# Kernel tuning notes

Measured on AMD Instinct MI355X. Metric: run time of the kernel, lower is better.

## Reference

```python
import jax, jax.numpy as jnp
import numpy as np

HEAD_DIM = 32
KERNEL = 3
DILATION = 2
PAD = DILATION * (KERNEL - 1) // 2  # 'same' padding for dilated window
SCALE = HEAD_DIM ** -0.5


def _unfold_windows(x):
    """x: [B, d, H, W] -> [B, d, k*k, H, W] dilated local windows.
    Matches torch nn.Unfold ordering: kernel row-major (i outer, j inner)."""
    B, d, H, W = x.shape
    xp = jnp.pad(x, ((0, 0), (0, 0), (PAD, PAD), (PAD, PAD)))
    taps = [xp[:, :, i * DILATION:i * DILATION + H, j * DILATION:j * DILATION + W]
            for i in range(KERNEL) for j in range(KERNEL)]  # fixed 9-tap loop
    return jnp.stack(taps, axis=2)


def setup_inputs() -> dict:
    key = jax.random.key(0)
    kq, kk, kv = jax.random.split(key, 3)
    shape = (16, 32, 128, 128)
    return {
        "q": jax.random.normal(kq, shape, dtype=jnp.float32),
        "k": jax.random.normal(kk, shape, dtype=jnp.float32),
        "v": jax.random.normal(kv, shape, dtype=jnp.float32),
    }


def reference(q, k, v):
    # k,v windows: [B, d, n, H, W] with n = kernel_size**2
    kw = _unfold_windows(k)
    vw = _unfold_windows(v)
    # per-pixel 1xN attention: scores [B, n, H, W]
    attn = jnp.einsum('bdhw,bdnhw->bnhw', q, kw) * SCALE
    attn = jax.nn.softmax(attn, axis=1)
    # weighted sum over window taps -> [B, d, H, W]
    return jnp.einsum('bnhw,bdnhw->bdhw', attn, vw)
```

## Files before the change

kernel.cpp:

```cpp
#include <hip/hip_runtime.h>


#define BB 16
#define HD 32
#define HH 128
#define WW 128
#define PLANE (HH * WW)
#define CHUNK 4

__global__ __launch_bounds__(128) void dilate_attn_kernel(
    const float* __restrict__ q,
    const float* __restrict__ k,
    const float* __restrict__ v,
    float* __restrict__ out)
{
    const int w   = threadIdx.x;
    const int bid = blockIdx.x;
    const int rowid = (bid & 7) * 256 + (bid >> 3);
    const int h = rowid & (HH - 1);
    const int b = rowid >> 7;

    const size_t base = ((size_t)b * HD) * PLANE + (size_t)h * WW + w;

    const int  dlo = (w >= 2)      ? -2      : -w;
    const int  dhi = (w <= WW - 3) ?  2      : (WW - 1 - w);
    const int  rlo = (h >= 2)      ? -2 * WW : 0;
    const int  rhi = (h <= HH - 3) ?  2 * WW : 0;
    const bool wlo = (w >= 2), whi = (w <= WW - 3);
    const bool hlo = (h >= 2), hhi = (h <= HH - 3);

    int off[9];
    off[0] = rlo + dlo; off[1] = rlo; off[2] = rlo + dhi;
    off[3] = dlo;       off[4] = 0;   off[5] = dhi;
    off[6] = rhi + dlo; off[7] = rhi; off[8] = rhi + dhi;

    const bool tv[9] = { hlo && wlo, hlo, hlo && whi,
                         wlo,        true, whi,
                         hhi && wlo, hhi, hhi && whi };

    float s[9];
    #pragma unroll
    for (int n = 0; n < 9; ++n) s[n] = 0.f;

    const float* qp = q + base;
    const float* kp = k + base;

    for (int dc = 0; dc < HD; dc += CHUNK) {
        float qreg[CHUNK];
        float kreg[CHUNK][9];
        #pragma unroll
        for (int u = 0; u < CHUNK; ++u) {
            const float* kc = kp + (size_t)(dc + u) * PLANE;
            qreg[u] = qp[(size_t)(dc + u) * PLANE];
            #pragma unroll
            for (int n = 0; n < 9; ++n) kreg[u][n] = kc[off[n]];
        }
        #pragma unroll
        for (int u = 0; u < CHUNK; ++u) {
            #pragma unroll
            for (int n = 0; n < 9; ++n)
                s[n] = fmaf(qreg[u], kreg[u][n], s[n]);
        }
    }

    #pragma unroll
    for (int n = 0; n < 9; ++n) if (!tv[n]) s[n] = 0.f;

    const float scale = 0.17677669529663687f;
    float m = -3.4e38f;
    #pragma unroll
    for (int n = 0; n < 9; ++n) { s[n] *= scale; m = fmaxf(m, s[n]); }
    float sum = 0.f;
    #pragma unroll
    for (int n = 0; n < 9; ++n) { s[n] = __expf(s[n] - m); sum += s[n]; }
    const float inv = 1.f / sum;
    #pragma unroll
    for (int n = 0; n < 9; ++n) s[n] *= inv;

    #pragma unroll
    for (int n = 0; n < 9; ++n) if (!tv[n]) s[n] = 0.f;

    const float* vp = v + base;
    float*       op = out + base;

    for (int dc = 0; dc < HD; dc += CHUNK) {
        float vreg[CHUNK][9];
        #pragma unroll
        for (int u = 0; u < CHUNK; ++u) {
            const float* vc = vp + (size_t)(dc + u) * PLANE;
            #pragma unroll
            for (int n = 0; n < 9; ++n) vreg[u][n] = vc[off[n]];
        }
        #pragma unroll
        for (int u = 0; u < CHUNK; ++u) {
            float acc = 0.f;
            #pragma unroll
            for (int n = 0; n < 9; ++n)
                acc = fmaf(s[n], vreg[u][n], acc);
            op[(size_t)(dc + u) * PLANE] = acc;
        }
    }
}

extern "C" void kernel_launch(void* const* d_in, const int* in_sizes, int n_in,
                              void* d_out, int out_size, void* d_ws, size_t ws_size,
                              hipStream_t stream) {
    const float* q = (const float*)d_in[0];
    const float* k = (const float*)d_in[1];
    const float* v = (const float*)d_in[2];
    float* out = (float*)d_out;

    dim3 grid(BB * HH);
    dim3 block(WW);
    dilate_attn_kernel<<<grid, block, 0, stream>>>(q, k, v, out);
}
```

Baseline: 34.31 us.

## Stage K/V row tiles in shared memory for multi-row blocks

Each block now handles four image rows with 512 threads and stages an 8-row halo strip of K and then V into LDS in channel chunks, using float4 global loads. Every thread reads its 9 window taps from shared memory, and Q is preloaded into registers for all channels. This replaces the many redundant global/L2 gathers per pixel, since the halo overlap is shared within a block. The cost is LDS traffic, two barriers per chunk and fewer, larger blocks (512 blocks in the grid). Halo rows outside the image are clamped and their taps masked as before.

Measured after the change: 33.25 us. -3.1%, faster.

```diff
diff --git a/kernel.cpp b/kernel.cpp
--- a/kernel.cpp
+++ b/kernel.cpp
@@ -6,61 +6,85 @@
 #define HH 128
 #define WW 128
 #define PLANE (HH * WW)
-#define CHUNK 4
+#define TH 4
+#define SR 8
+#define DC 8
+#define NCH (HD / DC)
+#define NT 512
 
-__global__ __launch_bounds__(128) void dilate_attn_kernel(
+__global__ __launch_bounds__(NT) void dilate_attn_kernel(
     const float* __restrict__ q,
     const float* __restrict__ k,
     const float* __restrict__ v,
     float* __restrict__ out)
 {
-    const int w   = threadIdx.x;
+    __shared__ float sm[DC * SR * WW];
+
+    const int tid = threadIdx.x;
     const int bid = blockIdx.x;
-    const int rowid = (bid & 7) * 256 + (bid >> 3);
-    const int h = rowid & (HH - 1);
-    const int b = rowid >> 7;
+    const int tile = (bid & 7) * 64 + (bid >> 3);
+    const int b  = tile >> 5;
+    const int r0 = (tile & 31) * TH;
 
-    const size_t base = ((size_t)b * HD) * PLANE + (size_t)h * WW + w;
+    const int lr = tid >> 7;
+    const int w  = tid & (WW - 1);
 
-    const int  dlo = (w >= 2)      ? -2      : -w;
-    const int  dhi = (w <= WW - 3) ?  2      : (WW - 1 - w);
-    const int  rlo = (h >= 2)      ? -2 * WW : 0;
-    const int  rhi = (h <= HH - 3) ?  2 * WW : 0;
+    const size_t bbase = (size_t)b * HD * PLANE;
+    const int pix = (r0 + lr) * WW + w;
+
+    const int  dlo = (w >= 2)      ? -2 : -w;
+    const int  dhi = (w <= WW - 3) ?  2 : (WW - 1 - w);
     const bool wlo = (w >= 2), whi = (w <= WW - 3);
+    const int  h   = r0 + lr;
     const bool hlo = (h >= 2), hhi = (h <= HH - 3);
-
-    int off[9];
-    off[0] = rlo + dlo; off[1] = rlo; off[2] = rlo + dhi;
-    off[3] = dlo;       off[4] = 0;   off[5] = dhi;
-    off[6] = rhi + dlo; off[7] = rhi; off[8] = rhi + dhi;
-
     const bool tv[9] = { hlo && wlo, hlo, hlo && whi,
                          wlo,        true, whi,
                          hhi && wlo, hhi, hhi && whi };
+
+    float qreg[HD];
+    #pragma unroll
+    for (int d = 0; d < HD; ++d)
+        qreg[d] = q[bbase + (size_t)d * PLANE + pix];
 
     float s[9];
     #pragma unroll
     for (int n = 0; n < 9; ++n) s[n] = 0.f;
 
-    const float* qp = q + base;
-    const float* kp = k + base;
-
-    for (int dc = 0; dc < HD; dc += CHUNK) {
-        float qreg[CHUNK];
-        float kreg[CHUNK][9];
+    for (int c = 0; c < NCH; ++c) {
+        {
+            float4 tmp[4];
+            int    la[4];
+            #pragma unroll
+            for (int j = 0; j < 4; ++j) {
+                const int i   = tid + j * NT;
+                const int u   = i >> 8;
+                const int rem = i & 255;
+                const int row = rem >> 5;
+                const int w4  = (rem & 31) << 2;
+                int gr = r0 - 2 + row;
+                gr = gr < 0 ? 0 : (gr > HH - 1 ? HH - 1 : gr);
+                tmp[j] = *(const float4*)(k + bbase + (size_t)(c * DC + u) * PLANE
+                                          + (size_t)gr * WW + w4);
+                la[j] = u * (SR * WW) + row * WW + w4;
+            }
+            #pragma unroll
+            for (int j = 0; j < 4; ++j)
+                *(float4*)(sm + la[j]) = tmp[j];
+        }
+        __syncthreads();
         #pragma unroll
-        for (int u = 0; u < CHUNK; ++u) {
-            const float* kc = kp + (size_t)(dc + u) * PLANE;
-            qreg[u] = qp[(size_t)(dc + u) * PLANE];
+        for (int u = 0; u < DC; ++u) {
+            const float  qd = qreg[c * DC + u];
+            const float* rp0 = sm + u * (SR * WW) + lr * WW + w;
             #pragma unroll
-            for (int n = 0; n < 9; ++n) kreg[u][n] = kc[off[n]];
+            for (int ti = 0; ti < 3; ++ti) {
+                const float* rp = rp0 + ti * 2 * WW;
+                s[ti * 3 + 0] = fmaf(qd, rp[dlo], s[ti * 3 + 0]);
+                s[ti * 3 + 1] = fmaf(qd, rp[0],   s[ti * 3 + 1]);
+                s[ti * 3 + 2] = fmaf(qd, rp[dhi], s[ti * 3 + 2]);
+            }
         }
-        #pragma unroll
-        for (int u = 0; u < CHUNK; ++u) {
-            #pragma unroll
-            for (int n = 0; n < 9; ++n)
-                s[n] = fmaf(qreg[u], kreg[u][n], s[n]);
-        }
+        __syncthreads();
     }
 
     #pragma unroll
@@ -80,25 +104,42 @@
     #pragma unroll
     for (int n = 0; n < 9; ++n) if (!tv[n]) s[n] = 0.f;
 
-    const float* vp = v + base;
-    float*       op = out + base;
-
-    for (int dc = 0; dc < HD; dc += CHUNK) {
-        float vreg[CHUNK][9];
+    for (int c = 0; c < NCH; ++c) {
+        {
+            float4 tmp[4];
+            int    la[4];
+            #pragma unroll
+            for (int j = 0; j < 4; ++j) {
+                const int i   = tid + j * NT;
+                const int u   = i >> 8;
+                const int rem = i & 255;
+                const int row = rem >> 5;
+                const int w4  = (rem & 31) << 2;
+                int gr = r0 - 2 + row;
+                gr = gr < 0 ? 0 : (gr > HH - 1 ? HH - 1 : gr);
+                tmp[j] = *(const float4*)(v + bbase + (size_t)(c * DC + u) * PLANE
+                                          + (size_t)gr * WW + w4);
+                la[j] = u * (SR * WW) + row * WW + w4;
+            }
+            #pragma unroll
+            for (int j = 0; j < 4; ++j)
+                *(float4*)(sm + la[j]) = tmp[j];
+        }
+        __syncthreads();
         #pragma unroll
-        for (int u = 0; u < CHUNK; ++u) {
-            const float* vc = vp + (size_t)(dc + u) * PLANE;
-            #pragma unroll
-            for (int n = 0; n < 9; ++n) vreg[u][n] = vc[off[n]];
-        }
-        #pragma unroll
-        for (int u = 0; u < CHUNK; ++u) {
+        for (int u = 0; u < DC; ++u) {
+            const float* rp0 = sm + u * (SR * WW) + lr * WW + w;
             float acc = 0.f;
             #pragma unroll
-            for (int n = 0; n < 9; ++n)
-                acc = fmaf(s[n], vreg[u][n], acc);
-            op[(size_t)(dc + u) * PLANE] = acc;
+            for (int ti = 0; ti < 3; ++ti) {
+                const float* rp = rp0 + ti * 2 * WW;
+                acc = fmaf(s[ti * 3 + 0], rp[dlo], acc);
+                acc = fmaf(s[ti * 3 + 1], rp[0],   acc);
+                acc = fmaf(s[ti * 3 + 2], rp[dhi], acc);
+            }
+            out[bbase + (size_t)(c * DC + u) * PLANE + pix] = acc;
         }
+        __syncthreads();
     }
 }
 
@@ -110,7 +151,7 @@
     const float* v = (const float*)d_in[2];
     float* out = (float*)d_out;
 
-    dim3 grid(BB * HH);
-    dim3 block(WW);
+    dim3 grid(BB * HH / TH);
+    dim3 block(NT);
     dilate_attn_kernel<<<grid, block, 0, stream>>>(q, k, v, out);
 }
```

## Process two pixels per thread with float2 loads and split head dim across half-waves

Applied to the files above, without the earlier changes.

Each thread now handles two adjacent pixels using float2 loads and stores for q, k, v and out. The 32-channel head dimension is split between the two half-waves of a 64-lane wavefront, and the partial scores are combined with a cross-lane xor shuffle. Each 256-thread block covers two rows, so the grid is halved. The aim is to cut the number of load instructions and the per-pixel address overhead in this memory-bound kernel, and to give each thread more independent work. In exchange it needs more registers per thread, and the shuffle adds a reduction step.

Result: slower. 48.55 us (+41.5%).

```diff
diff --git a/kernel.cpp b/kernel.cpp
--- a/kernel.cpp
+++ b/kernel.cpp
@@ -7,97 +7,134 @@
 #define WW 128
 #define PLANE (HH * WW)
 #define CHUNK 4
+#define HALF 16
 
-__global__ __launch_bounds__(128) void dilate_attn_kernel(
+__global__ __launch_bounds__(256, 4) void dilate_attn_kernel(
     const float* __restrict__ q,
     const float* __restrict__ k,
     const float* __restrict__ v,
     float* __restrict__ out)
 {
-    const int w   = threadIdx.x;
-    const int bid = blockIdx.x;
-    const int rowid = (bid & 7) * 256 + (bid >> 3);
+    const int tid   = threadIdx.x;
+    const int lane  = tid & 63;
+    const int dh    = lane >> 5;
+    const int wsub  = lane & 31;
+    const int wave  = tid >> 6;
+    const int lr    = wave >> 1;
+    const int whalf = wave & 1;
+    const int w2    = whalf * 64 + wsub * 2;
+
+    const int bid   = blockIdx.x;
+    const int tile  = (bid & 7) * 128 + (bid >> 3);
+    const int rowid = tile * 2 + lr;
     const int h = rowid & (HH - 1);
     const int b = rowid >> 7;
 
-    const size_t base = ((size_t)b * HD) * PLANE + (size_t)h * WW + w;
+    const size_t dbase = ((size_t)b * HD + (size_t)dh * HALF) * PLANE;
+    const int pix = h * WW + w2;
 
-    const int  dlo = (w >= 2)      ? -2      : -w;
-    const int  dhi = (w <= WW - 3) ?  2      : (WW - 1 - w);
-    const int  rlo = (h >= 2)      ? -2 * WW : 0;
-    const int  rhi = (h <= HH - 3) ?  2 * WW : 0;
-    const bool wlo = (w >= 2), whi = (w <= WW - 3);
+    const int dlo = (w2 >= 2)   ? -2      : 0;
+    const int dhi = (w2 <= 124) ?  2      : 0;
+    const int roff[3] = { (h >= 2) ? -2 * WW : 0, 0, (h <= HH - 3) ? 2 * WW : 0 };
     const bool hlo = (h >= 2), hhi = (h <= HH - 3);
+    const bool wlo0 = (w2 >= 2), wlo1 = (w2 >= 1);
+    const bool whi0 = (w2 <= 125), whi1 = (w2 <= 124);
+    const bool tv0[9] = { hlo && wlo0, hlo, hlo && whi0,
+                          wlo0,        true, whi0,
+                          hhi && wlo0, hhi, hhi && whi0 };
+    const bool tv1[9] = { hlo && wlo1, hlo, hlo && whi1,
+                          wlo1,        true, whi1,
+                          hhi && wlo1, hhi, hhi && whi1 };
 
-    int off[9];
-    off[0] = rlo + dlo; off[1] = rlo; off[2] = rlo + dhi;
-    off[3] = dlo;       off[4] = 0;   off[5] = dhi;
-    off[6] = rhi + dlo; off[7] = rhi; off[8] = rhi + dhi;
+    float s0[9], s1[9];
+    #pragma unroll
+    for (int n = 0; n < 9; ++n) { s0[n] = 0.f; s1[n] = 0.f; }
 
-    const bool tv[9] = { hlo && wlo, hlo, hlo && whi,
-                         wlo,        true, whi,
-                         hhi && wlo, hhi, hhi && whi };
+    const float* qp = q + dbase + pix;
+    const float* kp = k + dbase + pix;
 
-    float s[9];
-    #pragma unroll
-    for (int n = 0; n < 9; ++n) s[n] = 0.f;
-
-    const float* qp = q + base;
-    const float* kp = k + base;
-
-    for (int dc = 0; dc < HD; dc += CHUNK) {
-        float qreg[CHUNK];
-        float kreg[CHUNK][9];
+    #pragma unroll 1
+    for (int c = 0; c < HALF; c += CHUNK) {
+        float2 qreg[CHUNK], kreg[CHUNK][9];
         #pragma unroll
         for (int u = 0; u < CHUNK; ++u) {
-            const float* kc = kp + (size_t)(dc + u) * PLANE;
-            qreg[u] = qp[(size_t)(dc + u) * PLANE];
+            const float* kc = kp + (size_t)(c + u) * PLANE;
+            qreg[u] = *(const float2*)(qp + (size_t)(c + u) * PLANE);
             #pragma unroll
-            for (int n = 0; n < 9; ++n) kreg[u][n] = kc[off[n]];
+            for (int ti = 0; ti < 3; ++ti) {
+                const float* kr = kc + roff[ti];
+                kreg[u][ti * 3 + 0] = *(const float2*)(kr + dlo);
+                kreg[u][ti * 3 + 1] = *(const float2*)(kr);
+                kreg[u][ti * 3 + 2] = *(const float2*)(kr + dhi);
+            }
         }
         #pragma unroll
         for (int u = 0; u < CHUNK; ++u) {
             #pragma unroll
-            for (int n = 0; n < 9; ++n)
-                s[n] = fmaf(qreg[u], kreg[u][n], s[n]);
+            for (int n = 0; n < 9; ++n) {
+                s0[n] = fmaf(qreg[u].x, kreg[u][n].x, s0[n]);
+                s1[n] = fmaf(qreg[u].y, kreg[u][n].y, s1[n]);
+            }
         }
     }
 
     #pragma unroll
-    for (int n = 0; n < 9; ++n) if (!tv[n]) s[n] = 0.f;
+    for (int n = 0; n < 9; ++n) {
+        s0[n] += __shfl_xor(s0[n], 32);
+        s1[n] += __shfl_xor(s1[n], 32);
+    }
+
+    #pragma unroll
+    for (int n = 0; n < 9; ++n) { if (!tv0[n]) s0[n] = 0.f; if (!tv1[n]) s1[n] = 0.f; }
 
     const float scale = 0.17677669529663687f;
-    float m = -3.4e38f;
-    #pragma unroll
-    for (int n = 0; n < 9; ++n) { s[n] *= scale; m = fmaxf(m, s[n]); }
-    float sum = 0.f;
-    #pragma unroll
-    for (int n = 0; n < 9; ++n) { s[n] = __expf(s[n] - m); sum += s[n]; }
-    const float inv = 1.f / sum;
-    #pragma unroll
-    for (int n = 0; n < 9; ++n) s[n] *= inv;
+    {
+        float m0 = -3.4e38f, m1 = -3.4e38f;
+        #pragma unroll
+        for (int n = 0; n < 9; ++n) {
+            s0[n] *= scale; m0 = fmaxf(m0, s0[n]);
+            s1[n] *= scale; m1 = fmaxf(m1, s1[n]);
+        }
+        float sum0 = 0.f, sum1 = 0.f;
+        #pragma unroll
+        for (int n = 0; n < 9; ++n) {
+            s0[n] = __expf(s0[n] - m0); sum0 += s0[n];
+            s1[n] = __expf(s1[n] - m1); sum1 += s1[n];
+        }
+        const float i0 = 1.f / sum0, i1 = 1.f / sum1;
+        #pragma unroll
+        for (int n = 0; n < 9; ++n) { s0[n] *= i0; s1[n] *= i1; }
+    }
 
     #pragma unroll
-    for (int n = 0; n < 9; ++n) if (!tv[n]) s[n] = 0.f;
+    for (int n = 0; n < 9; ++n) { if (!tv0[n]) s0[n] = 0.f; if (!tv1[n]) s1[n] = 0.f; }
 
-    const float* vp = v + base;
-    float*       op = out + base;
+    const float* vp = v + dbase + pix;
+    float*       op = out + dbase + pix;
 
-    for (int dc = 0; dc < HD; dc += CHUNK) {
-        float vreg[CHUNK][9];
+    #pragma unroll 1
+    for (int c = 0; c < HALF; c += CHUNK) {
+        float2 vreg[CHUNK][9];
         #pragma unroll
         for (int u = 0; u < CHUNK; ++u) {
-            const float* vc = vp + (size_t)(dc + u) * PLANE;
+            const float* vc = vp + (size_t)(c + u) * PLANE;
             #pragma unroll
-            for (int n = 0; n < 9; ++n) vreg[u][n] = vc[off[n]];
+            for (int ti = 0; ti < 3; ++ti) {
+                const float* vr = vc + roff[ti];
+                vreg[u][ti * 3 + 0] = *(const float2*)(vr + dlo);
+                vreg[u][ti * 3 + 1] = *(const float2*)(vr);
+                vreg[u][ti * 3 + 2] = *(const float2*)(vr + dhi);
+            }
         }
         #pragma unroll
         for (int u = 0; u < CHUNK; ++u) {
-            float acc = 0.f;
+            float a0 = 0.f, a1 = 0.f;
             #pragma unroll
-            for (int n = 0; n < 9; ++n)
-                acc = fmaf(s[n], vreg[u][n], acc);
-            op[(size_t)(dc + u) * PLANE] = acc;
+            for (int n = 0; n < 9; ++n) {
+                a0 = fmaf(s0[n], vreg[u][n].x, a0);
+                a1 = fmaf(s1[n], vreg[u][n].y, a1);
+            }
+            *(float2*)(op + (size_t)(c + u) * PLANE) = make_float2(a0, a1);
         }
     }
 }
@@ -110,7 +147,7 @@
     const float* v = (const float*)d_in[2];
     float* out = (float*)d_out;
 
-    dim3 grid(BB * HH);
-    dim3 block(WW);
+    dim3 grid(BB * HH / 2);
+    dim3 block(256);
     dilate_attn_kernel<<<grid, block, 0, stream>>>(q, k, v, out);
 }
```

## Vectorize dilated attention with float4 per-thread pixel tiles and split head dim

Applied to the files above, without the earlier changes.

Each thread now handles four adjacent pixels using float4 loads of the three column windows per row tap, reusing loaded neighbors across pixels. The head dimension is split between the two halves of a wavefront and combined with a cross-lane shuffle. Blocks grow to 256 threads covering four rows. This cuts per-element load instruction count, but register pressure increases.

Result: slower. 40.05 us (+16.7%).

```diff
diff --git a/kernel.cpp b/kernel.cpp
--- a/kernel.cpp
+++ b/kernel.cpp
@@ -6,98 +6,163 @@
 #define HH 128
 #define WW 128
 #define PLANE (HH * WW)
-#define CHUNK 4
+#define CHUNK 2
+#define HALF 16
 
-__global__ __launch_bounds__(128) void dilate_attn_kernel(
+__global__ __launch_bounds__(256, 2) void dilate_attn_kernel(
     const float* __restrict__ q,
     const float* __restrict__ k,
     const float* __restrict__ v,
     float* __restrict__ out)
 {
-    const int w   = threadIdx.x;
-    const int bid = blockIdx.x;
-    const int rowid = (bid & 7) * 256 + (bid >> 3);
+    const int tid  = threadIdx.x;
+    const int lane = tid & 63;
+    const int wv   = tid >> 6;
+    const int dh   = lane >> 5;
+    const int lw   = lane & 31;
+    const int w4   = lw * 4;
+
+    const int bid   = blockIdx.x;
+    const int tile  = (bid & 7) * 64 + (bid >> 3);
+    const int rowid = tile * 4 + wv;
     const int h = rowid & (HH - 1);
     const int b = rowid >> 7;
 
-    const size_t base = ((size_t)b * HD) * PLANE + (size_t)h * WW + w;
+    const size_t dbase = ((size_t)b * HD + (size_t)dh * HALF) * PLANE;
+    const int rowbase = h * WW;
 
-    const int  dlo = (w >= 2)      ? -2      : -w;
-    const int  dhi = (w <= WW - 3) ?  2      : (WW - 1 - w);
-    const int  rlo = (h >= 2)      ? -2 * WW : 0;
-    const int  rhi = (h <= HH - 3) ?  2 * WW : 0;
-    const bool wlo = (w >= 2), whi = (w <= WW - 3);
     const bool hlo = (h >= 2), hhi = (h <= HH - 3);
+    const int roff[3] = { hlo ? -2 * WW : 0, 0, hhi ? 2 * WW : 0 };
 
-    int off[9];
-    off[0] = rlo + dlo; off[1] = rlo; off[2] = rlo + dhi;
-    off[3] = dlo;       off[4] = 0;   off[5] = dhi;
-    off[6] = rhi + dlo; off[7] = rhi; off[8] = rhi + dhi;
+    const int lo_c = (w4 >= 4)      ? w4 - 4 : 0;
+    const int hi_c = (w4 <= WW - 8) ? w4 + 4 : WW - 8;
 
-    const bool tv[9] = { hlo && wlo, hlo, hlo && whi,
-                         wlo,        true, whi,
-                         hhi && wlo, hhi, hhi && whi };
+    bool cvlo[4], cvhi[4];
+    #pragma unroll
+    for (int p = 0; p < 4; ++p) {
+        cvlo[p] = (w4 + p >= 2);
+        cvhi[p] = (w4 + p <= WW - 3);
+    }
 
-    float s[9];
+    float s[4][9];
     #pragma unroll
-    for (int n = 0; n < 9; ++n) s[n] = 0.f;
+    for (int p = 0; p < 4; ++p)
+        #pragma unroll
+        for (int n = 0; n < 9; ++n) s[p][n] = 0.f;
 
-    const float* qp = q + base;
-    const float* kp = k + base;
+    const float* qp = q + dbase + rowbase;
+    const float* kp = k + dbase + rowbase;
 
-    for (int dc = 0; dc < HD; dc += CHUNK) {
-        float qreg[CHUNK];
-        float kreg[CHUNK][9];
+    for (int c = 0; c < HALF; c += CHUNK) {
+        float4 qreg[CHUNK];
+        float4 kk[CHUNK][3][3];
         #pragma unroll
         for (int u = 0; u < CHUNK; ++u) {
-            const float* kc = kp + (size_t)(dc + u) * PLANE;
-            qreg[u] = qp[(size_t)(dc + u) * PLANE];
+            const float* kc = kp + (size_t)(c + u) * PLANE;
+            qreg[u] = *(const float4*)(qp + (size_t)(c + u) * PLANE + w4);
             #pragma unroll
-            for (int n = 0; n < 9; ++n) kreg[u][n] = kc[off[n]];
+            for (int ti = 0; ti < 3; ++ti) {
+                const float* kr = kc + roff[ti];
+                kk[u][ti][0] = *(const float4*)(kr + lo_c);
+                kk[u][ti][1] = *(const float4*)(kr + w4);
+                kk[u][ti][2] = *(const float4*)(kr + hi_c);
+            }
         }
         #pragma unroll
         for (int u = 0; u < CHUNK; ++u) {
+            const float qa[4] = { qreg[u].x, qreg[u].y, qreg[u].z, qreg[u].w };
             #pragma unroll
-            for (int n = 0; n < 9; ++n)
-                s[n] = fmaf(qreg[u], kreg[u][n], s[n]);
+            for (int ti = 0; ti < 3; ++ti) {
+                const float c12[12] = {
+                    kk[u][ti][0].x, kk[u][ti][0].y, kk[u][ti][0].z, kk[u][ti][0].w,
+                    kk[u][ti][1].x, kk[u][ti][1].y, kk[u][ti][1].z, kk[u][ti][1].w,
+                    kk[u][ti][2].x, kk[u][ti][2].y, kk[u][ti][2].z, kk[u][ti][2].w };
+                #pragma unroll
+                for (int p = 0; p < 4; ++p) {
+                    s[p][ti * 3 + 0] = fmaf(qa[p], c12[2 + p], s[p][ti * 3 + 0]);
+                    s[p][ti * 3 + 1] = fmaf(qa[p], c12[4 + p], s[p][ti * 3 + 1]);
+                    s[p][ti * 3 + 2] = fmaf(qa[p], c12[6 + p], s[p][ti * 3 + 2]);
+                }
+            }
         }
     }
 
     #pragma unroll
-    for (int n = 0; n < 9; ++n) if (!tv[n]) s[n] = 0.f;
+    for (int p = 0; p < 4; ++p)
+        #pragma unroll
+        for (int n = 0; n < 9; ++n)
+            s[p][n] += __shfl_xor(s[p][n], 32);
+
+    #pragma unroll
+    for (int p = 0; p < 4; ++p) {
+        const bool rv[3] = { hlo, true, hhi };
+        #pragma unroll
+        for (int ti = 0; ti < 3; ++ti) {
+            if (!(rv[ti] && cvlo[p])) s[p][ti * 3 + 0] = 0.f;
+            if (!rv[ti])              s[p][ti * 3 + 1] = 0.f;
+            if (!(rv[ti] && cvhi[p])) s[p][ti * 3 + 2] = 0.f;
+        }
+    }
 
     const float scale = 0.17677669529663687f;
-    float m = -3.4e38f;
     #pragma unroll
-    for (int n = 0; n < 9; ++n) { s[n] *= scale; m = fmaxf(m, s[n]); }
-    float sum = 0.f;
-    #pragma unroll
-    for (int n = 0; n < 9; ++n) { s[n] = __expf(s[n] - m); sum += s[n]; }
-    const float inv = 1.f / sum;
-    #pragma unroll
-    for (int n = 0; n < 9; ++n) s[n] *= inv;
+    for (int p = 0; p < 4; ++p) {
+        float m = -3.4e38f;
+        #pragma unroll
+        for (int n = 0; n < 9; ++n) { s[p][n] *= scale; m = fmaxf(m, s[p][n]); }
+        float sum = 0.f;
+        #pragma unroll
+        for (int n = 0; n < 9; ++n) { s[p][n] = __expf(s[p][n] - m); sum += s[p][n]; }
+        const float inv = 1.f / sum;
+        #pragma unroll
+        for (int n = 0; n < 9; ++n) s[p][n] *= inv;
+    }
 
     #pragma unroll
-    for (int n = 0; n < 9; ++n) if (!tv[n]) s[n] = 0.f;
+    for (int p = 0; p < 4; ++p) {
+        const bool rv[3] = { hlo, true, hhi };
+        #pragma unroll
+        for (int ti = 0; ti < 3; ++ti) {
+            if (!(rv[ti] && cvlo[p])) s[p][ti * 3 + 0] = 0.f;
+            if (!rv[ti])              s[p][ti * 3 + 1] = 0.f;
+            if (!(rv[ti] && cvhi[p])) s[p][ti * 3 + 2] = 0.f;
+        }
+    }
 
-    const float* vp = v + base;
-    float*       op = out + base;
+    const float* vp = v + dbase + rowbase;
+    float*       op = out + dbase + rowbase;
 
-    for (int dc = 0; dc < HD; dc += CHUNK) {
-        float vreg[CHUNK][9];
+    for (int c = 0; c < HALF; c += CHUNK) {
+        float4 vv[CHUNK][3][3];
         #pragma unroll
         for (int u = 0; u < CHUNK; ++u) {
-            const float* vc = vp + (size_t)(dc + u) * PLANE;
+            const float* vc = vp + (size_t)(c + u) * PLANE;
             #pragma unroll
-            for (int n = 0; n < 9; ++n) vreg[u][n] = vc[off[n]];
+            for (int ti = 0; ti < 3; ++ti) {
+                const float* vr = vc + roff[ti];
+                vv[u][ti][0] = *(const float4*)(vr + lo_c);
+                vv[u][ti][1] = *(const float4*)(vr + w4);
+                vv[u][ti][2] = *(const float4*)(vr + hi_c);
+            }
         }
         #pragma unroll
         for (int u = 0; u < CHUNK; ++u) {
-            float acc = 0.f;
+            float a[4] = { 0.f, 0.f, 0.f, 0.f };
             #pragma unroll
-            for (int n = 0; n < 9; ++n)
-                acc = fmaf(s[n], vreg[u][n], acc);
-            op[(size_t)(dc + u) * PLANE] = acc;
+            for (int ti = 0; ti < 3; ++ti) {
+                const float c12[12] = {
+                    vv[u][ti][0].x, vv[u][ti][0].y, vv[u][ti][0].z, vv[u][ti][0].w,
+                    vv[u][ti][1].x, vv[u][ti][1].y, vv[u][ti][1].z, vv[u][ti][1].w,
+                    vv[u][ti][2].x, vv[u][ti][2].y, vv[u][ti][2].z, vv[u][ti][2].w };
+                #pragma unroll
+                for (int p = 0; p < 4; ++p) {
+                    a[p] = fmaf(s[p][ti * 3 + 0], c12[2 + p], a[p]);
+                    a[p] = fmaf(s[p][ti * 3 + 1], c12[4 + p], a[p]);
+                    a[p] = fmaf(s[p][ti * 3 + 2], c12[6 + p], a[p]);
+                }
+            }
+            *(float4*)(op + (size_t)(c + u) * PLANE + w4) =
+                make_float4(a[0], a[1], a[2], a[3]);
         }
     }
 }
@@ -110,7 +175,7 @@
     const float* v = (const float*)d_in[2];
     float* out = (float*)d_out;
 
-    dim3 grid(BB * HH);
-    dim3 block(WW);
+    dim3 grid(BB * HH / 4);
+    dim3 block(256);
     dilate_attn_kernel<<<grid, block, 0, stream>>>(q, k, v, out);
 }
```
